# Optimization experiments

Measured on AMD Instinct MI355X. Metric: run time of the kernel, lower is better.

## Reference

```python
import jax, jax.numpy as jnp
import numpy as np


def _conv(x, w, b):
    # PyTorch Conv2d(k=4, s=2, p=1): NCHW x OIHW correlation
    y = jax.lax.conv_general_dilated(x, w, window_strides=(2, 2),
                                     padding=((1, 1), (1, 1)),
                                     dimension_numbers=('NCHW', 'OIHW', 'NCHW'))
    return y + b[None, :, None, None]


def _conv_t(x, w, b):
    # PyTorch ConvTranspose2d(k=4, s=2, p=1); w has torch shape (Cin, Cout, 4, 4).
    # Adjoint of strided correlation = correlation with spatially-flipped,
    # channel-swapped kernel and lhs dilation; pad = k - 1 - p = 2.
    wk = jnp.flip(w, (2, 3)).transpose(1, 0, 2, 3)  # (Cout, Cin, 4, 4)
    y = jax.lax.conv_general_dilated(x, wk, window_strides=(1, 1),
                                     padding=((2, 2), (2, 2)),
                                     lhs_dilation=(2, 2),
                                     dimension_numbers=('NCHW', 'OIHW', 'NCHW'))
    return y + b[None, :, None, None]


def setup_inputs() -> dict:
    key = jax.random.key(0)
    ks = jax.random.split(key, 18)
    s = 0.05
    inp = {'x': jax.random.normal(ks[0], (32, 3, 256, 256), jnp.float32)}
    # encoder weights (OIHW)
    enc_shapes = [(64, 3, 4, 4), (128, 64, 4, 4), (256, 128, 4, 4), (512, 256, 4, 4)]
    for i, sh in enumerate(enc_shapes):
        inp[f'e_w{i+1}'] = jax.random.normal(ks[1 + i], sh, jnp.float32) * s
        inp[f'e_b{i+1}'] = jnp.zeros((sh[0],), jnp.float32)
    # decoder weights (torch ConvTranspose2d layout: Cin, Cout, kH, kW)
    dec_shapes = [(512, 128, 4, 4), (128, 64, 4, 4), (64, 32, 4, 4), (32, 3, 4, 4)]
    for i, sh in enumerate(dec_shapes):
        inp[f'd_w{i+1}'] = jax.random.normal(ks[5 + i], sh, jnp.float32) * s
        inp[f'd_b{i+1}'] = jnp.zeros((sh[1],), jnp.float32)
    # codebook (num_embeddings=1024, embedding_dim=512)
    inp['embed'] = jax.random.normal(ks[9], (1024, 512), jnp.float32)
    return inp


def reference(x, e_w1, e_b1, e_w2, e_b2, e_w3, e_b3, e_w4, e_b4,
              d_w1, d_b1, d_w2, d_b2, d_w3, d_b3, d_w4, d_b4, embed):
    # encoder
    h = jax.nn.relu(_conv(x, e_w1, e_b1))
    h = jax.nn.relu(_conv(h, e_w2, e_b2))
    h = jax.nn.relu(_conv(h, e_w3, e_b3))
    z = jax.nn.relu(_conv(h, e_w4, e_b4))  # (B, 512, 16, 16)
    # quantizer: NCHW -> NHWC -> flat (B*H*W, D)
    B, D, H, W = z.shape
    z_flat = z.transpose(0, 2, 3, 1).reshape(-1, D)
    # squared L2 distance to each code: ||z||^2 - 2 z.E^T + ||E||^2
    dist = (jnp.sum(z_flat ** 2, axis=1, keepdims=True)
            - 2.0 * z_flat @ embed.T
            + jnp.sum(embed ** 2, axis=1))  # (N, K)
    idx = jnp.argmin(dist, axis=1)
    quantized = embed[idx]  # gather == one_hot @ embed
    z_q = quantized.reshape(B, H, W, D).transpose(0, 3, 1, 2)  # NCHW
    # decoder
    h = jax.nn.relu(_conv_t(z_q, d_w1, d_b1))
    h = jax.nn.relu(_conv_t(h, d_w2, d_b2))
    h = jax.nn.relu(_conv_t(h, d_w3, d_b3))
    out = jnp.tanh(_conv_t(h, d_w4, d_b4))  # (B, 3, 256, 256)
    return out
```

## Files before the change

kernel.cpp:

```cpp
#include <hip/hip_runtime.h>
#include <math.h>


typedef __attribute__((ext_vector_type(8))) short bf16x8;
typedef __attribute__((ext_vector_type(4))) float f32x4;
union FragU { unsigned u[4]; bf16x8 v; };

__device__ __forceinline__ unsigned bf16_rne(unsigned u) {
    return (u + 0x7FFFu + ((u >> 16) & 1u)) >> 16;
}
__device__ __forceinline__ unsigned pack_split(float v) {
    unsigned u = __builtin_bit_cast(unsigned, v);
    unsigned hi = bf16_rne(u);
    float hif = __builtin_bit_cast(float, hi << 16);
    float r = v - hif;
    unsigned lo = bf16_rne(__builtin_bit_cast(unsigned, r));
    return hi | (lo << 16);
}

__global__ void __launch_bounds__(256) pack_tensor(
    const float* __restrict__ s, unsigned* __restrict__ d, int n)
{
    int i = blockIdx.x * 256 + threadIdx.x;
    if (i < n) d[i] = pack_split(s[i]);
}

template<int Cin, int Cout>
__global__ void __launch_bounds__(256) repack_wt(
    const float* __restrict__ w, unsigned* __restrict__ wq)
{
    constexpr int TOT = 16 * Cin * Cout;
    int idx = blockIdx.x * 256 + threadIdx.x;
    if (idx >= TOT) return;
    int t  = idx & 3;
    int ci = (idx >> 2) % Cin;
    int rest = (idx >> 2) / Cin;
    int co  = rest % Cout;
    int par = rest / Cout;
    int dy = par >> 1, dx = par & 1;
    int r = t >> 1, s = t & 1;
    int ky = 3 - dy - 2 * r;
    int kx = 3 - dx - 2 * s;
    float v = w[(((size_t)ci * Cout + co) * 4 + ky) * 4 + kx];
    wq[idx] = pack_split(v);
}

__global__ void __launch_bounds__(256) embed_transpose(
    const float* __restrict__ embed, float* __restrict__ et)
{
    int idx = blockIdx.x * 256 + threadIdx.x;
    int c = idx & 1023, k = idx >> 10;
    et[idx] = embed[(size_t)c * 512 + k];
}

template<int Cin, int H, int W, int Cout, int PACKO>
__global__ void __launch_bounds__(256) conv4s2_mfma(
    const unsigned* __restrict__ xp, const unsigned* __restrict__ wp,
    const float* __restrict__ bias, float* __restrict__ y)
{
    constexpr int OH = H / 2, OW = W / 2;
    constexpr int LOG_OW = (OW == 64) ? 6 : (OW == 32) ? 5 : 4;
    constexpr int R   = 64 / OW;
    constexpr int RT  = 2 * R + 2;
    constexpr int CS  = W + 2;
    constexpr int XEL = 2 * RT * CS;
    constexpr int XIT = (XEL + 255) / 256;
    constexpr int K   = Cin * 16;
    constexpr int NC  = Cin / 2;
    constexpr int NB  = 128;
    constexpr int MBC = 32 * OH * OW / 64;

    __shared__ unsigned smem[8704];
    unsigned* raw = smem;
    unsigned* wb  = smem + ((XEL + 7) & ~7);

    int bid = blockIdx.x;
    int mb = bid % MBC, ng = bid / MBC;
    int oc0 = ng * NB;
    int m0 = mb * 64;
    int nimg = m0 / (OH * OW);
    int sp0 = m0 % (OH * OW);
    int oyb = sp0 >> LOG_OW;

    int tid  = threadIdx.x;
    int lane = tid & 63, wv = tid >> 6;
    int lm = lane & 15, q = lane >> 4;
    int n0w = wv * 32;

    const unsigned* xbase = xp + (size_t)nimg * Cin * H * W;

    int  goff[XIT];
    bool gok[XIT];
#pragma unroll
    for (int s = 0; s < XIT; ++s) {
        int i = tid + 256 * s;
        goff[s] = 0; gok[s] = false;
        if (i < XEL) {
            int lc = i % CS;
            int t2 = i / CS;
            int lr = t2 % RT;
            int c  = t2 / RT;
            int gr = 2 * oyb - 1 + lr;
            int gc = lc - 1;
            bool ok = ((unsigned)gr < (unsigned)H) && ((unsigned)gc < (unsigned)W);
            goff[s] = ok ? (c * H * W + gr * W + gc) : 0;
            gok[s]  = ok;
        }
    }
    const unsigned* wbase = wp + (size_t)(oc0 + (tid >> 5)) * K + (tid & 31);
    int wlds0 = (tid >> 5) * 36 + (tid & 31);

    f32x4 acc[4][2];
#pragma unroll
    for (int nt = 0; nt < 2; ++nt) {
        float b = bias[oc0 + n0w + nt * 16 + lm];
#pragma unroll
        for (int mt = 0; mt < 4; ++mt)
#pragma unroll
            for (int r = 0; r < 4; ++r) acc[mt][nt][r] = b;
    }

    unsigned pfa[XIT];
    unsigned pfb[16];

    auto load_chunk = [&](int ch) {
        const unsigned* cb = xbase + (size_t)(ch * 2) * (H * W);
#pragma unroll
        for (int s = 0; s < XIT; ++s) {
            unsigned v = 0;
            if (gok[s]) v = cb[goff[s]];
            pfa[s] = v;
        }
        const unsigned* wc = wbase + ch * 32;
#pragma unroll
        for (int s = 0; s < 16; ++s) pfb[s] = wc[(size_t)s * 8 * K];
    };
    auto store_chunk = [&]() {
#pragma unroll
        for (int s = 0; s < XIT; ++s) {
            int i = tid + 256 * s;
            if (i < XEL) raw[i] = pfa[s];
        }
#pragma unroll
        for (int s = 0; s < 16; ++s) wb[wlds0 + s * 288] = pfb[s];
    };

    load_chunk(0);
#pragma unroll 1
    for (int ch = 0; ch < NC; ++ch) {
        __syncthreads();
        store_chunk();
        __syncthreads();
        if (ch + 1 < NC) load_chunk(ch + 1);

        FragU bhi[2], blo[2];
#pragma unroll
        for (int nt = 0; nt < 2; ++nt) {
            const unsigned* bp = &wb[(n0w + nt * 16 + lm) * 36 + q * 8];
            uint4 p0 = *(const uint4*)bp;
            uint4 p1 = *(const uint4*)(bp + 4);
            unsigned e0 = p0.x, e1 = p0.y, e2 = p0.z, e3 = p0.w;
            unsigned e4 = p1.x, e5 = p1.y, e6 = p1.z, e7 = p1.w;
            bhi[nt].u[0] = (e0 & 0xffffu) | (e1 << 16);
            bhi[nt].u[1] = (e2 & 0xffffu) | (e3 << 16);
            bhi[nt].u[2] = (e4 & 0xffffu) | (e5 << 16);
            bhi[nt].u[3] = (e6 & 0xffffu) | (e7 << 16);
            blo[nt].u[0] = (e0 >> 16) | (e1 & 0xffff0000u);
            blo[nt].u[1] = (e2 >> 16) | (e3 & 0xffff0000u);
            blo[nt].u[2] = (e4 >> 16) | (e5 & 0xffff0000u);
            blo[nt].u[3] = (e6 >> 16) | (e7 & 0xffff0000u);
        }
#pragma unroll
        for (int mt = 0; mt < 4; ++mt) {
            int m = mt * 16 + lm;
            int oyl = m >> LOG_OW, oxl = m & (OW - 1);
            int c = q >> 1, rb = 2 * oyl + (q & 1) * 2;
            const unsigned* rp = &raw[(c * RT + rb) * CS + 2 * oxl];
            uint2 a0 = *(const uint2*)rp;
            uint2 a1 = *(const uint2*)(rp + 2);
            uint2 a2 = *(const uint2*)(rp + CS);
            uint2 a3 = *(const uint2*)(rp + CS + 2);
            FragU ahi, alo;
            ahi.u[0] = (a0.x & 0xffffu) | (a0.y << 16);
            ahi.u[1] = (a1.x & 0xffffu) | (a1.y << 16);
            ahi.u[2] = (a2.x & 0xffffu) | (a2.y << 16);
            ahi.u[3] = (a3.x & 0xffffu) | (a3.y << 16);
            alo.u[0] = (a0.x >> 16) | (a0.y & 0xffff0000u);
            alo.u[1] = (a1.x >> 16) | (a1.y & 0xffff0000u);
            alo.u[2] = (a2.x >> 16) | (a2.y & 0xffff0000u);
            alo.u[3] = (a3.x >> 16) | (a3.y & 0xffff0000u);
#pragma unroll
            for (int nt = 0; nt < 2; ++nt) {
                acc[mt][nt] = __builtin_amdgcn_mfma_f32_16x16x32_bf16(
                    ahi.v, bhi[nt].v, acc[mt][nt], 0, 0, 0);
                acc[mt][nt] = __builtin_amdgcn_mfma_f32_16x16x32_bf16(
                    ahi.v, blo[nt].v, acc[mt][nt], 0, 0, 0);
                acc[mt][nt] = __builtin_amdgcn_mfma_f32_16x16x32_bf16(
                    alo.v, bhi[nt].v, acc[mt][nt], 0, 0, 0);
            }
        }
    }

    __syncthreads();
    float* cs = (float*)smem;
#pragma unroll
    for (int mt = 0; mt < 4; ++mt)
#pragma unroll
        for (int nt = 0; nt < 2; ++nt) {
            int nl = n0w + nt * 16 + lm;
#pragma unroll
            for (int r = 0; r < 4; ++r)
                cs[nl * 68 + mt * 16 + q * 4 + r] = acc[mt][nt][r];
        }
    __syncthreads();
    {
        int nl = tid >> 1, half = tid & 1;
        size_t gb = ((size_t)(nimg * Cout + oc0 + nl)) * (OH * OW) + sp0 + half * 32;
#pragma unroll
        for (int i2 = 0; i2 < 8; ++i2) {
            float4 v = *(float4*)&cs[nl * 68 + half * 32 + 4 * i2];
            v.x = fmaxf(v.x, 0.0f); v.y = fmaxf(v.y, 0.0f);
            v.z = fmaxf(v.z, 0.0f); v.w = fmaxf(v.w, 0.0f);
            if (PACKO) {
                uint4 p;
                p.x = pack_split(v.x); p.y = pack_split(v.y);
                p.z = pack_split(v.z); p.w = pack_split(v.w);
                *(uint4*)((unsigned*)y + gb + 4 * i2) = p;
            } else {
                *(float4*)(y + gb + 4 * i2) = v;
            }
        }
    }
}

template<int Cin, int Hh, int Wh, int Cout, int MT, int NT, int PACKO>
__global__ void __launch_bounds__(256) convt4s2_mfma(
    const unsigned* __restrict__ xp, const unsigned* __restrict__ wq,
    const float* __restrict__ bias, float* __restrict__ y)
{
    constexpr int W = Wh;
    constexpr int LOG_W = (W == 64) ? 6 : (W == 32) ? 5 : 4;
    constexpr int R   = 64 / W;
    constexpr int RT  = R + 1;
    constexpr int CS  = W + 2;
    constexpr int XEL = 8 * RT * CS;
    constexpr int XIT = (XEL + 255) / 256;
    constexpr int K   = Cin * 4;
    constexpr int NC  = Cin / 8;
    constexpr int NB  = Cout;
    constexpr int WIT = NB / 8;
    constexpr int WN  = Cout / (16 * NT);
    constexpr int WM  = 4 / WN;
    static_assert(WM * MT * 16 == 64, "M tiling");
    static_assert(WN * NT * 16 == Cout, "N tiling");
    constexpr int MBC = 32 * Hh * W / 64;
    constexpr int XPAD = (XEL + 7) & ~7;
    constexpr int SM1 = XPAD + NB * 36;
    constexpr int SM2 = NB * 68;
    constexpr int SMEM = SM1 > SM2 ? SM1 : SM2;

    __shared__ unsigned smem[SMEM];
    unsigned* raw = smem;
    unsigned* wb  = smem + XPAD;

    int bid = blockIdx.x;
    int mb  = bid % MBC;
    int par = bid / MBC;
    int dy = par >> 1, dx = par & 1;

    int m0   = mb * 64;
    int nimg = m0 / (Hh * W);
    int sp0  = m0 % (Hh * W);
    int il0  = sp0 >> LOG_W;

    int tid = threadIdx.x;
    int lane = tid & 63, wv = tid >> 6;
    int lm = lane & 15, q = lane >> 4;
    int wm = wv / WN, wn = wv % WN;

    const unsigned* xbase = xp + (size_t)nimg * Cin * Hh * W;

    int  goff[XIT];
    bool gok[XIT];
#pragma unroll
    for (int s = 0; s < XIT; ++s) {
        int i = tid + 256 * s;
        goff[s] = 0; gok[s] = false;
        if (i < XEL) {
            int lc = i % CS;
            int t2 = i / CS;
            int lr = t2 % RT;
            int c  = t2 / RT;
            int gr = il0 - 1 + dy + lr;
            int gc = lc - 1;
            bool ok = ((unsigned)gr < (unsigned)Hh) && ((unsigned)gc < (unsigned)W);
            goff[s] = ok ? (c * Hh * W + gr * W + gc) : 0;
            gok[s]  = ok;
        }
    }
    const unsigned* wbase = wq + (size_t)(par * Cout + (tid >> 5)) * K + (tid & 31);
    int wlds0 = (tid >> 5) * 36 + (tid & 31);

    f32x4 acc[MT][NT];
#pragma unroll
    for (int nt = 0; nt < NT; ++nt) {
        float b = bias[wn * NT * 16 + nt * 16 + lm];
#pragma unroll
        for (int mt = 0; mt < MT; ++mt)
#pragma unroll
            for (int r = 0; r < 4; ++r) acc[mt][nt][r] = b;
    }

    unsigned pfa[XIT];
    unsigned pfb[WIT];

    auto load_chunk = [&](int ch) {
        const unsigned* cb = xbase + (size_t)(ch * 8) * (Hh * W);
#pragma unroll
        for (int s = 0; s < XIT; ++s) {
            unsigned v = 0;
            if (gok[s]) v = cb[goff[s]];
            pfa[s] = v;
        }
        const unsigned* wc = wbase + ch * 32;
#pragma unroll
        for (int s = 0; s < WIT; ++s) pfb[s] = wc[(size_t)s * 8 * K];
    };
    auto store_chunk = [&]() {
#pragma unroll
        for (int s = 0; s < XIT; ++s) {
            int i = tid + 256 * s;
            if (i < XEL) raw[i] = pfa[s];
        }
#pragma unroll
        for (int s = 0; s < WIT; ++s) wb[wlds0 + s * 288] = pfb[s];
    };

    load_chunk(0);
#pragma unroll 1
    for (int ch = 0; ch < NC; ++ch) {
        __syncthreads();
        store_chunk();
        __syncthreads();
        if (ch + 1 < NC) load_chunk(ch + 1);

        FragU bhi[NT], blo[NT];
#pragma unroll
        for (int nt = 0; nt < NT; ++nt) {
            const unsigned* bp = &wb[(wn * NT * 16 + nt * 16 + lm) * 36 + q * 8];
            uint4 p0 = *(const uint4*)bp;
            uint4 p1 = *(const uint4*)(bp + 4);
            unsigned e0 = p0.x, e1 = p0.y, e2 = p0.z, e3 = p0.w;
            unsigned e4 = p1.x, e5 = p1.y, e6 = p1.z, e7 = p1.w;
            bhi[nt].u[0] = (e0 & 0xffffu) | (e1 << 16);
            bhi[nt].u[1] = (e2 & 0xffffu) | (e3 << 16);
            bhi[nt].u[2] = (e4 & 0xffffu) | (e5 << 16);
            bhi[nt].u[3] = (e6 & 0xffffu) | (e7 << 16);
            blo[nt].u[0] = (e0 >> 16) | (e1 & 0xffff0000u);
            blo[nt].u[1] = (e2 >> 16) | (e3 & 0xffff0000u);
            blo[nt].u[2] = (e4 >> 16) | (e5 & 0xffff0000u);
            blo[nt].u[3] = (e6 >> 16) | (e7 & 0xffff0000u);
        }
#pragma unroll
        for (int mt = 0; mt < MT; ++mt) {
            int ml = wm * (MT * 16) + mt * 16 + lm;
            int il = ml >> LOG_W, jl = ml & (W - 1);
            const unsigned* rp = &raw[((2 * q) * RT + il) * CS + jl + dx];
            unsigned a00 = rp[0],               a01 = rp[1];
            unsigned a10 = rp[CS],              a11 = rp[CS + 1];
            unsigned a20 = rp[RT * CS],         a21 = rp[RT * CS + 1];
            unsigned a30 = rp[RT * CS + CS],    a31 = rp[RT * CS + CS + 1];
            FragU ahi, alo;
            ahi.u[0] = (a00 & 0xffffu) | (a01 << 16);
            ahi.u[1] = (a10 & 0xffffu) | (a11 << 16);
            ahi.u[2] = (a20 & 0xffffu) | (a21 << 16);
            ahi.u[3] = (a30 & 0xffffu) | (a31 << 16);
            alo.u[0] = (a00 >> 16) | (a01 & 0xffff0000u);
            alo.u[1] = (a10 >> 16) | (a11 & 0xffff0000u);
            alo.u[2] = (a20 >> 16) | (a21 & 0xffff0000u);
            alo.u[3] = (a30 >> 16) | (a31 & 0xffff0000u);
#pragma unroll
            for (int nt = 0; nt < NT; ++nt) {
                acc[mt][nt] = __builtin_amdgcn_mfma_f32_16x16x32_bf16(
                    ahi.v, bhi[nt].v, acc[mt][nt], 0, 0, 0);
                acc[mt][nt] = __builtin_amdgcn_mfma_f32_16x16x32_bf16(
                    ahi.v, blo[nt].v, acc[mt][nt], 0, 0, 0);
                acc[mt][nt] = __builtin_amdgcn_mfma_f32_16x16x32_bf16(
                    alo.v, bhi[nt].v, acc[mt][nt], 0, 0, 0);
            }
        }
    }

    __syncthreads();
    float* cs = (float*)smem;
#pragma unroll
    for (int mt = 0; mt < MT; ++mt)
#pragma unroll
        for (int nt = 0; nt < NT; ++nt) {
            int nl  = wn * NT * 16 + nt * 16 + lm;
            int mb2 = wm * (MT * 16) + mt * 16 + q * 4;
#pragma unroll
            for (int r = 0; r < 4; ++r)
                cs[nl * 68 + mb2 + r] = acc[mt][nt][r];
        }
    __syncthreads();
    constexpr int EIT = NB * 64 / 256;
#pragma unroll
    for (int it = 0; it < EIT; ++it) {
        int idx = tid + 256 * it;
        int c = idx >> 6, m = idx & 63;
        int il = m >> LOG_W, jl = m & (W - 1);
        int oy = 2 * (il0 + il) + dy;
        int ox = 2 * jl + dx;
        float v = fmaxf(cs[c * 68 + m], 0.0f);
        size_t go = (((size_t)(nimg * Cout + c)) * (2 * Hh) + oy) * (2 * W) + ox;
        if (PACKO) ((unsigned*)y)[go] = pack_split(v);
        else       y[go] = v;
    }
}

template<int Cin, int H, int W, int OCT, int UNR, bool INT>
__device__ __forceinline__ void conv_core(
    const float* __restrict__ xn, const float* __restrict__ wbase,
    int iy0, int ix0, float (&acc)[OCT][4])
{
#pragma unroll UNR
    for (int ic = 0; ic < Cin; ++ic) {
        const float* xc = xn + (size_t)ic * (H * W);
        float xv[4][10];
#pragma unroll
        for (int ky = 0; ky < 4; ++ky) {
            int iy = iy0 + ky;
            if (INT) {
                const float* xr = xc + (size_t)iy * W;
#pragma unroll
                for (int j = 0; j < 10; ++j) xv[ky][j] = xr[ix0 + j];
            } else {
                bool rv = ((unsigned)iy < (unsigned)H);
                const float* xr = xc + (size_t)(rv ? iy : 0) * W;
#pragma unroll
                for (int j = 0; j < 10; ++j) {
                    int ix = ix0 + j;
                    bool cv = rv && ((unsigned)ix < (unsigned)W);
                    xv[ky][j] = cv ? xr[cv ? ix : 0] : 0.0f;
                }
            }
        }
#pragma unroll
        for (int o = 0; o < OCT; ++o) {
            const float* wr = wbase + (size_t)o * (Cin * 16) + ic * 16;
#pragma unroll
            for (int ky = 0; ky < 4; ++ky) {
                float w0 = wr[ky * 4 + 0], w1 = wr[ky * 4 + 1];
                float w2 = wr[ky * 4 + 2], w3 = wr[ky * 4 + 3];
#pragma unroll
                for (int j = 0; j < 4; ++j) {
                    acc[o][j] = fmaf(xv[ky][2 * j],     w0, acc[o][j]);
                    acc[o][j] = fmaf(xv[ky][2 * j + 1], w1, acc[o][j]);
                    acc[o][j] = fmaf(xv[ky][2 * j + 2], w2, acc[o][j]);
                    acc[o][j] = fmaf(xv[ky][2 * j + 3], w3, acc[o][j]);
                }
            }
        }
    }
}

template<int Cin, int H, int W, int Cout, int OCT, int UNR, int PACKO>
__global__ void __launch_bounds__(256) conv4s2_k(
    const float* __restrict__ x, const float* __restrict__ w,
    const float* __restrict__ bias, float* __restrict__ y)
{
    constexpr int OH = H / 2, OW = W / 2, OWq = OW / 4;
    int id = blockIdx.x * 256 + threadIdx.x;
    int ox4 = id % OWq; int t = id / OWq;
    int oy  = t % OH;   t /= OH;
    int ocg = t % (Cout / OCT);
    int n   = t / (Cout / OCT);
    int oc0 = __builtin_amdgcn_readfirstlane(ocg * OCT);
    n       = __builtin_amdgcn_readfirstlane(n);

    float acc[OCT][4];
#pragma unroll
    for (int o = 0; o < OCT; ++o) {
        float b = bias[oc0 + o];
#pragma unroll
        for (int j = 0; j < 4; ++j) acc[o][j] = b;
    }

    const float* xn    = x + (size_t)n * Cin * H * W;
    const float* wbase = w + (size_t)oc0 * Cin * 16;
    int iy0 = 2 * oy - 1;
    int ix0 = 8 * ox4 - 1;

    bool interior = (oy >= 1) && (oy <= OH - 2) && (ox4 >= 1) && (ox4 <= OWq - 2);
    if (interior) conv_core<Cin, H, W, OCT, UNR, true >(xn, wbase, iy0, ix0, acc);
    else          conv_core<Cin, H, W, OCT, UNR, false>(xn, wbase, iy0, ix0, acc);

    int ox0 = ox4 * 4;
#pragma unroll
    for (int o = 0; o < OCT; ++o) {
        size_t gb = (((size_t)n * Cout + oc0 + o) * OH + oy) * OW + ox0;
#pragma unroll
        for (int j = 0; j < 4; ++j) {
            float v = fmaxf(acc[o][j], 0.0f);
            if (PACKO) ((unsigned*)y)[gb + j] = pack_split(v);
            else       y[gb + j] = v;
        }
    }
}

template<int Cin, int H, int W, int Cout, int COT, int ACT, int UNR>
__global__ void __launch_bounds__(256) convt4s2_k(
    const float* __restrict__ x, const float* __restrict__ w,
    const float* __restrict__ bias, float* __restrict__ y)
{
    constexpr int OH = 2 * H, OW = 2 * W, OWq = OW / 4;
    int id = blockIdx.x * 256 + threadIdx.x;
    int ox4 = id % OWq; int t = id / OWq;
    int oy  = t % OH;   t /= OH;
    int cog = t % (Cout / COT);
    int n   = t / (Cout / COT);
    int co0 = __builtin_amdgcn_readfirstlane(cog * COT);
    n       = __builtin_amdgcn_readfirstlane(n);

    int p   = (oy + 1) & 1;
    int iyA = (oy + 1 - p) >> 1;
    int iyB = iyA - 1;
    bool vA = (iyA < H);
    bool vB = (iyB >= 0);
    int iyAc = vA ? iyA : 0, iyBc = vB ? iyB : 0;

    int t0 = 2 * ox4;
    bool c0 = (t0 - 1 >= 0);
    bool c3 = (t0 + 2 <= W - 1);
    int j0 = c0 ? t0 - 1 : 0;
    int j3 = c3 ? t0 + 2 : 0;

    float acc[COT][4];
#pragma unroll
    for (int o = 0; o < COT; ++o) {
        float b = bias[co0 + o];
#pragma unroll
        for (int j = 0; j < 4; ++j) acc[o][j] = b;
    }

    const float* xn = x + (size_t)n * Cin * H * W;

#pragma unroll UNR
    for (int ci = 0; ci < Cin; ++ci) {
        const float* xc  = xn + (size_t)ci * (H * W);
        const float* xrA = xc + (size_t)iyAc * W;
        const float* xrB = xc + (size_t)iyBc * W;
        float a0 = (vA && c0) ? xrA[j0]     : 0.0f;
        float a1 =  vA        ? xrA[t0]     : 0.0f;
        float a2 =  vA        ? xrA[t0 + 1] : 0.0f;
        float a3 = (vA && c3) ? xrA[j3]     : 0.0f;
        float b0 = (vB && c0) ? xrB[j0]     : 0.0f;
        float b1 =  vB        ? xrB[t0]     : 0.0f;
        float b2 =  vB        ? xrB[t0 + 1] : 0.0f;
        float b3 = (vB && c3) ? xrB[j3]     : 0.0f;

        const float* wci = w + ((size_t)ci * Cout + co0) * 16;
#pragma unroll
        for (int o = 0; o < COT; ++o) {
            const float* wr = wci + (size_t)o * 16;
            float wA0 = wr[p * 4 + 0], wA1 = wr[p * 4 + 1];
            float wA2 = wr[p * 4 + 2], wA3 = wr[p * 4 + 3];
            float wB0 = wr[(p + 2) * 4 + 0], wB1 = wr[(p + 2) * 4 + 1];
            float wB2 = wr[(p + 2) * 4 + 2], wB3 = wr[(p + 2) * 4 + 3];
            acc[o][0] = fmaf(a1, wA1, acc[o][0]); acc[o][0] = fmaf(a0, wA3, acc[o][0]);
            acc[o][0] = fmaf(b1, wB1, acc[o][0]); acc[o][0] = fmaf(b0, wB3, acc[o][0]);
            acc[o][1] = fmaf(a2, wA0, acc[o][1]); acc[o][1] = fmaf(a1, wA2, acc[o][1]);
            acc[o][1] = fmaf(b2, wB0, acc[o][1]); acc[o][1] = fmaf(b1, wB2, acc[o][1]);
            acc[o][2] = fmaf(a2, wA1, acc[o][2]); acc[o][2] = fmaf(a1, wA3, acc[o][2]);
            acc[o][2] = fmaf(b2, wB1, acc[o][2]); acc[o][2] = fmaf(b1, wB3, acc[o][2]);
            acc[o][3] = fmaf(a3, wA0, acc[o][3]); acc[o][3] = fmaf(a2, wA2, acc[o][3]);
            acc[o][3] = fmaf(b3, wB0, acc[o][3]); acc[o][3] = fmaf(b2, wB2, acc[o][3]);
        }
    }

    int ox0 = ox4 * 4;
#pragma unroll
    for (int o = 0; o < COT; ++o) {
        float* yr = y + (((size_t)n * Cout + co0 + o) * OH + oy) * OW + ox0;
#pragma unroll
        for (int j = 0; j < 4; ++j) {
            float v = acc[o][j];
            yr[j] = (ACT == 0) ? fmaxf(v, 0.0f) : tanhf(v);
        }
    }
}

__global__ void __launch_bounds__(256) embed_norms(
    const float* __restrict__ embed, float* __restrict__ norms)
{
    int c = blockIdx.x * 256 + threadIdx.x;
    const float* e = embed + (size_t)c * 512;
    float s = 0.0f;
    for (int k = 0; k < 512; ++k) s = fmaf(e[k], e[k], s);
    norms[c] = s;
}

__global__ void __launch_bounds__(256) vq_argmin16(
    const float* __restrict__ z, const float* __restrict__ et,
    const float* __restrict__ norms, int* __restrict__ out)
{
    constexpr int ZS = 516;
    int row0 = blockIdx.x * 16;
    int n    = row0 >> 8;
    int yx0  = row0 & 255;
    int tid  = threadIdx.x;

    __shared__ float zr[16 * ZS];

    const float* zn = z + ((size_t)n * 512) * 256;
#pragma unroll
    for (int it = 0; it < 8; ++it) {
        int i  = tid + 256 * it;
        int rq = i & 3, kc = i >> 2;
        float4 v = *(const float4*)&zn[(size_t)kc * 256 + yx0 + 4 * rq];
        zr[(4 * rq + 0) * ZS + kc] = v.x;
        zr[(4 * rq + 1) * ZS + kc] = v.y;
        zr[(4 * rq + 2) * ZS + kc] = v.z;
        zr[(4 * rq + 3) * ZS + kc] = v.w;
    }
    __syncthreads();

    float acc[16][4];
#pragma unroll
    for (int r = 0; r < 16; ++r)
#pragma unroll
        for (int j = 0; j < 4; ++j) acc[r][j] = 0.0f;

    const float* ebase = et + 4 * tid;
#pragma unroll 1
    for (int k4 = 0; k4 < 128; ++k4) {
        float4 e0 = *(const float4*)&ebase[(size_t)(4 * k4 + 0) * 1024];
        float4 e1 = *(const float4*)&ebase[(size_t)(4 * k4 + 1) * 1024];
        float4 e2 = *(const float4*)&ebase[(size_t)(4 * k4 + 2) * 1024];
        float4 e3 = *(const float4*)&ebase[(size_t)(4 * k4 + 3) * 1024];
#pragma unroll
        for (int r = 0; r < 16; ++r) {
            float4 zz = *(const float4*)&zr[r * ZS + 4 * k4];
            float a0 = acc[r][0], a1 = acc[r][1], a2 = acc[r][2], a3 = acc[r][3];
            a0 = fmaf(zz.x, e0.x, a0); a0 = fmaf(zz.y, e1.x, a0);
            a0 = fmaf(zz.z, e2.x, a0); a0 = fmaf(zz.w, e3.x, a0);
            a1 = fmaf(zz.x, e0.y, a1); a1 = fmaf(zz.y, e1.y, a1);
            a1 = fmaf(zz.z, e2.y, a1); a1 = fmaf(zz.w, e3.y, a1);
            a2 = fmaf(zz.x, e0.z, a2); a2 = fmaf(zz.y, e1.z, a2);
            a2 = fmaf(zz.z, e2.z, a2); a2 = fmaf(zz.w, e3.z, a2);
            a3 = fmaf(zz.x, e0.w, a3); a3 = fmaf(zz.y, e1.w, a3);
            a3 = fmaf(zz.z, e2.w, a3); a3 = fmaf(zz.w, e3.w, a3);
            acc[r][0] = a0; acc[r][1] = a1; acc[r][2] = a2; acc[r][3] = a3;
        }
    }

    float4 nb = *(const float4*)&norms[4 * tid];
    float best[16]; int bi[16];
#pragma unroll
    for (int r = 0; r < 16; ++r) {
        float d0 = nb.x - 2.0f * acc[r][0];
        float d1 = nb.y - 2.0f * acc[r][1];
        float d2 = nb.z - 2.0f * acc[r][2];
        float d3 = nb.w - 2.0f * acc[r][3];
        float b = d0; int ix = 4 * tid;
        if (d1 < b) { b = d1; ix = 4 * tid + 1; }
        if (d2 < b) { b = d2; ix = 4 * tid + 2; }
        if (d3 < b) { b = d3; ix = 4 * tid + 3; }
        best[r] = b; bi[r] = ix;
    }

    __syncthreads();
    float* rbd = zr;
    int*   rbi = (int*)(zr + 4096);
#pragma unroll
    for (int r = 0; r < 16; ++r) {
        rbd[r * 256 + tid] = best[r];
        rbi[r * 256 + tid] = bi[r];
    }
    __syncthreads();
    for (int s = 128; s > 0; s >>= 1) {
        if (tid < s) {
#pragma unroll
            for (int r = 0; r < 16; ++r) {
                int i0 = r * 256 + tid;
                float od = rbd[i0 + s]; int oi = rbi[i0 + s];
                float md = rbd[i0];     int mi = rbi[i0];
                if (od < md || (od == md && oi < mi)) { rbd[i0] = od; rbi[i0] = oi; }
            }
        }
        __syncthreads();
    }
    if (tid < 16) out[row0 + tid] = rbi[tid * 256];
}

__global__ void __launch_bounds__(256) vq_gather_pack(
    const int* __restrict__ vidx, const float* __restrict__ embed,
    unsigned* __restrict__ zq)
{
    int i = blockIdx.x * 256 + threadIdx.x;
    int yx = i & 255;
    int t  = i >> 8;
    int c  = t & 511;
    int n  = t >> 9;
    int row = (n << 8) + yx;
    zq[i] = pack_split(embed[(size_t)vidx[row] * 512 + c]);
}

extern "C" void kernel_launch(void* const* d_in, const int* in_sizes, int n_in,
                              void* d_out, int out_size, void* d_ws, size_t ws_size,
                              hipStream_t stream)
{
    (void)in_sizes; (void)n_in; (void)out_size; (void)ws_size;
    const float* x     = (const float*)d_in[0];
    const float* ew1   = (const float*)d_in[1];
    const float* eb1   = (const float*)d_in[2];
    const float* ew2   = (const float*)d_in[3];
    const float* eb2   = (const float*)d_in[4];
    const float* ew3   = (const float*)d_in[5];
    const float* eb3   = (const float*)d_in[6];
    const float* ew4   = (const float*)d_in[7];
    const float* eb4   = (const float*)d_in[8];
    const float* dw1   = (const float*)d_in[9];
    const float* db1   = (const float*)d_in[10];
    const float* dw2   = (const float*)d_in[11];
    const float* db2   = (const float*)d_in[12];
    const float* dw3   = (const float*)d_in[13];
    const float* db3   = (const float*)d_in[14];
    const float* dw4   = (const float*)d_in[15];
    const float* db4   = (const float*)d_in[16];
    const float* embed = (const float*)d_in[17];
    float* out = (float*)d_out;

    unsigned* W0   = (unsigned*)d_ws;
    unsigned* h1p  = W0;
    unsigned* h2p  = W0 + 33554432;
    unsigned* h3p  = W0;
    float*    z    = (float*)(W0 + 8388608);
    unsigned* zq   = W0 + 12582912;
    float*    P0   = (float*)(W0 + 16777216);
    float*    P1   = (float*)(W0 + 20971520);
    int*      vidx = (int*)(W0 + 29360128);
    float*    norms= (float*)(W0 + 29368320);
    float*    g3o  = (float*)h2p;

    unsigned* wp2 = (unsigned*)d_out;
    unsigned* wp3 = wp2 + 131072;
    unsigned* wp4 = wp2 + 655360;
    unsigned* wq1 = wp2 + 2752512;
    unsigned* wq2 = wq1 + 1048576;
    unsigned* wq3 = wq2 + 131072;
    float*    et  = (float*)(wq3 + 32768);

    dim3 b256(256);

    pack_tensor<<<dim3(512),  b256, 0, stream>>>(ew2, wp2, 131072);
    pack_tensor<<<dim3(2048), b256, 0, stream>>>(ew3, wp3, 524288);
    pack_tensor<<<dim3(8192), b256, 0, stream>>>(ew4, wp4, 2097152);
    repack_wt<512, 128><<<dim3(4096), b256, 0, stream>>>(dw1, wq1);
    repack_wt<128,  64><<<dim3(512),  b256, 0, stream>>>(dw2, wq2);
    repack_wt< 64,  32><<<dim3(128),  b256, 0, stream>>>(dw3, wq3);
    embed_transpose<<<dim3(2048), b256, 0, stream>>>(embed, et);

    conv4s2_k<3, 256, 256, 64, 4, 3, 1><<<dim3(8192), b256, 0, stream>>>(
        x, ew1, eb1, (float*)h1p);
    conv4s2_mfma<64, 128, 128, 128, 1><<<dim3(2048), b256, 0, stream>>>(
        h1p, wp2, eb2, (float*)h2p);
    conv4s2_mfma<128, 64, 64, 256, 1><<<dim3(1024), b256, 0, stream>>>(
        h2p, wp3, eb3, (float*)h3p);
    conv4s2_mfma<256, 32, 32, 512, 0><<<dim3(512), b256, 0, stream>>>(
        h3p, wp4, eb4, z);

    embed_norms<<<dim3(4), b256, 0, stream>>>(embed, norms);
    vq_argmin16<<<dim3(512), b256, 0, stream>>>(z, et, norms, vidx);
    vq_gather_pack<<<dim3(16384), b256, 0, stream>>>(vidx, embed, zq);

    convt4s2_mfma<512, 16, 16, 128, 4, 2, 1><<<dim3(4 * 128), b256, 0, stream>>>(
        zq, wq1, db1, P0);
    convt4s2_mfma<128, 32, 32, 64, 4, 1, 1><<<dim3(4 * 512), b256, 0, stream>>>(
        (const unsigned*)P0, wq2, db2, P1);
    convt4s2_mfma<64, 64, 64, 32, 2, 1, 0><<<dim3(4 * 2048), b256, 0, stream>>>(
        (const unsigned*)P1, wq3, db3, g3o);
    convt4s2_k<32, 128, 128, 3, 3, 1, 2><<<dim3(2048), b256, 0, stream>>>(
        g3o, dw4, db4, out);
}
```

Baseline: 1.272 ms.

## Run first encoder conv on MFMA with split-bf16 packed input

Replaces the scalar FMA first encoder convolution (Cin=3) with a generalized MFMA implicit-GEMM kernel that pads Cin to 4, packs the input image and weights into hi/lo bf16 pairs, and uses three bf16 MFMAs per tile to approximate fp32. This aims to move the large 256x256 first layer onto matrix cores instead of vector ALUs. It adds an extra full-input packing pass over x and wastes a quarter of the K dimension on zero padding.

```diff
diff --git a/kernel.cpp b/kernel.cpp
--- a/kernel.cpp
+++ b/kernel.cpp
@@ -23,6 +23,16 @@
 {
     int i = blockIdx.x * 256 + threadIdx.x;
     if (i < n) d[i] = pack_split(s[i]);
+}
+
+__global__ void __launch_bounds__(256) pack_w1(
+    const float* __restrict__ w, unsigned* __restrict__ wq)
+{
+    int idx = blockIdx.x * 256 + threadIdx.x;
+    if (idx >= 64 * 64) return;
+    int k = idx & 63, oc = idx >> 6;
+    float v = (k < 48) ? w[oc * 48 + k] : 0.0f;
+    wq[idx] = pack_split(v);
 }
 
 template<int Cin, int Cout>
@@ -219,6 +229,204 @@
 #pragma unroll
         for (int i2 = 0; i2 < 8; ++i2) {
             float4 v = *(float4*)&cs[nl * 68 + half * 32 + 4 * i2];
+            v.x = fmaxf(v.x, 0.0f); v.y = fmaxf(v.y, 0.0f);
+            v.z = fmaxf(v.z, 0.0f); v.w = fmaxf(v.w, 0.0f);
+            if (PACKO) {
+                uint4 p;
+                p.x = pack_split(v.x); p.y = pack_split(v.y);
+                p.z = pack_split(v.z); p.w = pack_split(v.w);
+                *(uint4*)((unsigned*)y + gb + 4 * i2) = p;
+            } else {
+                *(float4*)(y + gb + 4 * i2) = v;
+            }
+        }
+    }
+}
+
+template<int Cin, int CINR, int H, int W, int Cout, int MT, int NT, int PACKO>
+__global__ void __launch_bounds__(256) conv4s2_mfma_g(
+    const unsigned* __restrict__ xp, const unsigned* __restrict__ wp,
+    const float* __restrict__ bias, float* __restrict__ y)
+{
+    constexpr int OH = H / 2, OW = W / 2;
+    constexpr int OWB = (OW >= 64) ? 64 : OW;
+    constexpr int LOG_OWB = (OWB == 64) ? 6 : (OWB == 32) ? 5 : 4;
+    constexpr int LOG_OW  = (OW == 128) ? 7 : (OW == 64) ? 6 : (OW == 32) ? 5 : 4;
+    constexpr int R   = 64 / OWB;
+    constexpr int RT  = 2 * R + 2;
+    constexpr int CS  = 2 * OWB + 2;
+    constexpr int XEL = 2 * RT * CS;
+    constexpr int XIT = (XEL + 255) / 256;
+    constexpr int K   = Cin * 16;
+    constexpr int NC  = Cin / 2;
+    constexpr int NB  = Cout;
+    constexpr int WIT = NB / 8;
+    constexpr int WN  = Cout / (16 * NT);
+    constexpr int WM  = 4 / WN;
+    static_assert(WM * MT * 16 == 64, "M tiling");
+    static_assert(WN * NT * 16 == Cout, "N tiling");
+    constexpr int MBC = 32 * OH * OW / 64;
+    constexpr int XPAD = (XEL + 7) & ~7;
+    constexpr int SM1 = XPAD + NB * 36;
+    constexpr int SM2 = NB * 68;
+    constexpr int SMEM = SM1 > SM2 ? SM1 : SM2;
+
+    __shared__ unsigned smem[SMEM];
+    unsigned* raw = smem;
+    unsigned* wb  = smem + XPAD;
+
+    int bid = blockIdx.x;
+    int mb = bid % MBC, ng = bid / MBC;
+    int oc0 = ng * NB;
+    int m0 = mb * 64;
+    int nimg = m0 / (OH * OW);
+    int sp0 = m0 % (OH * OW);
+    int oyb = sp0 >> LOG_OW;
+    int oxb = sp0 & (OW - 1);
+
+    int tid  = threadIdx.x;
+    int lane = tid & 63, wv = tid >> 6;
+    int lm = lane & 15, q = lane >> 4;
+    int wm = wv / WN, wn = wv % WN;
+
+    const unsigned* xbase = xp + (size_t)nimg * CINR * H * W;
+
+    int  goff[XIT];
+    bool gok[XIT];
+    int  cidx[XIT];
+#pragma unroll
+    for (int s = 0; s < XIT; ++s) {
+        int i = tid + 256 * s;
+        goff[s] = 0; gok[s] = false; cidx[s] = 0;
+        if (i < XEL) {
+            int lc = i % CS;
+            int t2 = i / CS;
+            int lr = t2 % RT;
+            int c  = t2 / RT;
+            int gr = 2 * oyb - 1 + lr;
+            int gc = 2 * oxb - 1 + lc;
+            bool ok = ((unsigned)gr < (unsigned)H) && ((unsigned)gc < (unsigned)W);
+            goff[s] = ok ? (c * H * W + gr * W + gc) : 0;
+            gok[s]  = ok;
+            cidx[s] = c;
+        }
+    }
+    const unsigned* wbase = wp + (size_t)(oc0 + (tid >> 5)) * K + (tid & 31);
+    int wlds0 = (tid >> 5) * 36 + (tid & 31);
+
+    f32x4 acc[MT][NT];
+#pragma unroll
+    for (int nt = 0; nt < NT; ++nt) {
+        float b = bias[oc0 + wn * NT * 16 + nt * 16 + lm];
+#pragma unroll
+        for (int mt = 0; mt < MT; ++mt)
+#pragma unroll
+            for (int r = 0; r < 4; ++r) acc[mt][nt][r] = b;
+    }
+
+    unsigned pfa[XIT];
+    unsigned pfb[WIT];
+
+    auto load_chunk = [&](int ch) {
+        const unsigned* cb = xbase + (size_t)(ch * 2) * (H * W);
+#pragma unroll
+        for (int s = 0; s < XIT; ++s) {
+            unsigned v = 0;
+            bool okc = (2 * ch + cidx[s]) < CINR;
+            if (gok[s] && okc) v = cb[goff[s]];
+            pfa[s] = v;
+        }
+        const unsigned* wc = wbase + ch * 32;
+#pragma unroll
+        for (int s = 0; s < WIT; ++s) pfb[s] = wc[(size_t)s * 8 * K];
+    };
+    auto store_chunk = [&]() {
+#pragma unroll
+        for (int s = 0; s < XIT; ++s) {
+            int i = tid + 256 * s;
+            if (i < XEL) raw[i] = pfa[s];
+        }
+#pragma unroll
+        for (int s = 0; s < WIT; ++s) wb[wlds0 + s * 288] = pfb[s];
+    };
+
+    load_chunk(0);
+#pragma unroll 1
+    for (int ch = 0; ch < NC; ++ch) {
+        __syncthreads();
+        store_chunk();
+        __syncthreads();
+        if (ch + 1 < NC) load_chunk(ch + 1);
+
+        FragU bhi[NT], blo[NT];
+#pragma unroll
+        for (int nt = 0; nt < NT; ++nt) {
+            const unsigned* bp = &wb[(wn * NT * 16 + nt * 16 + lm) * 36 + q * 8];
+            uint4 p0 = *(const uint4*)bp;
+            uint4 p1 = *(const uint4*)(bp + 4);
+            unsigned e0 = p0.x, e1 = p0.y, e2 = p0.z, e3 = p0.w;
+            unsigned e4 = p1.x, e5 = p1.y, e6 = p1.z, e7 = p1.w;
+            bhi[nt].u[0] = (e0 & 0xffffu) | (e1 << 16);
+            bhi[nt].u[1] = (e2 & 0xffffu) | (e3 << 16);
+            bhi[nt].u[2] = (e4 & 0xffffu) | (e5 << 16);
+            bhi[nt].u[3] = (e6 & 0xffffu) | (e7 << 16);
+            blo[nt].u[0] = (e0 >> 16) | (e1 & 0xffff0000u);
+            blo[nt].u[1] = (e2 >> 16) | (e3 & 0xffff0000u);
+            blo[nt].u[2] = (e4 >> 16) | (e5 & 0xffff0000u);
+            blo[nt].u[3] = (e6 >> 16) | (e7 & 0xffff0000u);
+        }
+#pragma unroll
+        for (int mt = 0; mt < MT; ++mt) {
+            int m = wm * (MT * 16) + mt * 16 + lm;
+            int oyl = m >> LOG_OWB, oxl = m & (OWB - 1);
+            int c = q >> 1, rb = 2 * oyl + (q & 1) * 2;
+            const unsigned* rp = &raw[(c * RT + rb) * CS + 2 * oxl];
+            uint2 a0 = *(const uint2*)rp;
+            uint2 a1 = *(const uint2*)(rp + 2);
+            uint2 a2 = *(const uint2*)(rp + CS);
+            uint2 a3 = *(const uint2*)(rp + CS + 2);
+            FragU ahi, alo;
+            ahi.u[0] = (a0.x & 0xffffu) | (a0.y << 16);
+            ahi.u[1] = (a1.x & 0xffffu) | (a1.y << 16);
+            ahi.u[2] = (a2.x & 0xffffu) | (a2.y << 16);
+            ahi.u[3] = (a3.x & 0xffffu) | (a3.y << 16);
+            alo.u[0] = (a0.x >> 16) | (a0.y & 0xffff0000u);
+            alo.u[1] = (a1.x >> 16) | (a1.y & 0xffff0000u);
+            alo.u[2] = (a2.x >> 16) | (a2.y & 0xffff0000u);
+            alo.u[3] = (a3.x >> 16) | (a3.y & 0xffff0000u);
+#pragma unroll
+            for (int nt = 0; nt < NT; ++nt) {
+                acc[mt][nt] = __builtin_amdgcn_mfma_f32_16x16x32_bf16(
+                    ahi.v, bhi[nt].v, acc[mt][nt], 0, 0, 0);
+                acc[mt][nt] = __builtin_amdgcn_mfma_f32_16x16x32_bf16(
+                    ahi.v, blo[nt].v, acc[mt][nt], 0, 0, 0);
+                acc[mt][nt] = __builtin_amdgcn_mfma_f32_16x16x32_bf16(
+                    alo.v, bhi[nt].v, acc[mt][nt], 0, 0, 0);
+            }
+        }
+    }
+
+    __syncthreads();
+    float* cs = (float*)smem;
+#pragma unroll
+    for (int mt = 0; mt < MT; ++mt)
+#pragma unroll
+        for (int nt = 0; nt < NT; ++nt) {
+            int nl  = wn * NT * 16 + nt * 16 + lm;
+            int mb2 = wm * (MT * 16) + mt * 16 + q * 4;
+#pragma unroll
+            for (int r = 0; r < 4; ++r)
+                cs[nl * 68 + mb2 + r] = acc[mt][nt][r];
+        }
+    __syncthreads();
+    {
+        constexpr int QT = 256 / NB;
+        int nl = tid / QT, qt = tid % QT;
+        constexpr int MQ = 64 / QT;
+        size_t gb = ((size_t)(nimg * Cout + oc0 + nl)) * (OH * OW) + sp0 + qt * MQ;
+#pragma unroll
+        for (int i2 = 0; i2 < MQ / 4; ++i2) {
+            float4 v = *(float4*)&cs[nl * 68 + qt * MQ + 4 * i2];
             v.x = fmaxf(v.x, 0.0f); v.y = fmaxf(v.y, 0.0f);
             v.z = fmaxf(v.z, 0.0f); v.w = fmaxf(v.w, 0.0f);
             if (PACKO) {
@@ -419,96 +627,6 @@
     }
 }
 
-template<int Cin, int H, int W, int OCT, int UNR, bool INT>
-__device__ __forceinline__ void conv_core(
-    const float* __restrict__ xn, const float* __restrict__ wbase,
-    int iy0, int ix0, float (&acc)[OCT][4])
-{
-#pragma unroll UNR
-    for (int ic = 0; ic < Cin; ++ic) {
-        const float* xc = xn + (size_t)ic * (H * W);
-        float xv[4][10];
-#pragma unroll
-        for (int ky = 0; ky < 4; ++ky) {
-            int iy = iy0 + ky;
-            if (INT) {
-                const float* xr = xc + (size_t)iy * W;
-#pragma unroll
-                for (int j = 0; j < 10; ++j) xv[ky][j] = xr[ix0 + j];
-            } else {
-                bool rv = ((unsigned)iy < (unsigned)H);
-                const float* xr = xc + (size_t)(rv ? iy : 0) * W;
-#pragma unroll
-                for (int j = 0; j < 10; ++j) {
-                    int ix = ix0 + j;
-                    bool cv = rv && ((unsigned)ix < (unsigned)W);
-                    xv[ky][j] = cv ? xr[cv ? ix : 0] : 0.0f;
-                }
-            }
-        }
-#pragma unroll
-        for (int o = 0; o < OCT; ++o) {
-            const float* wr = wbase + (size_t)o * (Cin * 16) + ic * 16;
-#pragma unroll
-            for (int ky = 0; ky < 4; ++ky) {
-                float w0 = wr[ky * 4 + 0], w1 = wr[ky * 4 + 1];
-                float w2 = wr[ky * 4 + 2], w3 = wr[ky * 4 + 3];
-#pragma unroll
-                for (int j = 0; j < 4; ++j) {
-                    acc[o][j] = fmaf(xv[ky][2 * j],     w0, acc[o][j]);
-                    acc[o][j] = fmaf(xv[ky][2 * j + 1], w1, acc[o][j]);
-                    acc[o][j] = fmaf(xv[ky][2 * j + 2], w2, acc[o][j]);
-                    acc[o][j] = fmaf(xv[ky][2 * j + 3], w3, acc[o][j]);
-                }
-            }
-        }
-    }
-}
-
-template<int Cin, int H, int W, int Cout, int OCT, int UNR, int PACKO>
-__global__ void __launch_bounds__(256) conv4s2_k(
-    const float* __restrict__ x, const float* __restrict__ w,
-    const float* __restrict__ bias, float* __restrict__ y)
-{
-    constexpr int OH = H / 2, OW = W / 2, OWq = OW / 4;
-    int id = blockIdx.x * 256 + threadIdx.x;
-    int ox4 = id % OWq; int t = id / OWq;
-    int oy  = t % OH;   t /= OH;
-    int ocg = t % (Cout / OCT);
-    int n   = t / (Cout / OCT);
-    int oc0 = __builtin_amdgcn_readfirstlane(ocg * OCT);
-    n       = __builtin_amdgcn_readfirstlane(n);
-
-    float acc[OCT][4];
-#pragma unroll
-    for (int o = 0; o < OCT; ++o) {
-        float b = bias[oc0 + o];
-#pragma unroll
-        for (int j = 0; j < 4; ++j) acc[o][j] = b;
-    }
-
-    const float* xn    = x + (size_t)n * Cin * H * W;
-    const float* wbase = w + (size_t)oc0 * Cin * 16;
-    int iy0 = 2 * oy - 1;
-    int ix0 = 8 * ox4 - 1;
-
-    bool interior = (oy >= 1) && (oy <= OH - 2) && (ox4 >= 1) && (ox4 <= OWq - 2);
-    if (interior) conv_core<Cin, H, W, OCT, UNR, true >(xn, wbase, iy0, ix0, acc);
-    else          conv_core<Cin, H, W, OCT, UNR, false>(xn, wbase, iy0, ix0, acc);
-
-    int ox0 = ox4 * 4;
-#pragma unroll
-    for (int o = 0; o < OCT; ++o) {
-        size_t gb = (((size_t)n * Cout + oc0 + o) * OH + oy) * OW + ox0;
-#pragma unroll
-        for (int j = 0; j < 4; ++j) {
-            float v = fmaxf(acc[o][j], 0.0f);
-            if (PACKO) ((unsigned*)y)[gb + j] = pack_split(v);
-            else       y[gb + j] = v;
-        }
-    }
-}
-
 template<int Cin, int H, int W, int Cout, int COT, int ACT, int UNR>
 __global__ void __launch_bounds__(256) convt4s2_k(
     const float* __restrict__ x, const float* __restrict__ w,
@@ -735,6 +853,7 @@
     unsigned* W0   = (unsigned*)d_ws;
     unsigned* h1p  = W0;
     unsigned* h2p  = W0 + 33554432;
+    unsigned* xp1  = W0 + 33554432;
     unsigned* h3p  = W0;
     float*    z    = (float*)(W0 + 8388608);
     unsigned* zq   = W0 + 12582912;
@@ -751,19 +870,22 @@
     unsigned* wq2 = wq1 + 1048576;
     unsigned* wq3 = wq2 + 131072;
     float*    et  = (float*)(wq3 + 32768);
+    unsigned* wp1 = (unsigned*)(et + 524288);
 
     dim3 b256(256);
 
     pack_tensor<<<dim3(512),  b256, 0, stream>>>(ew2, wp2, 131072);
     pack_tensor<<<dim3(2048), b256, 0, stream>>>(ew3, wp3, 524288);
     pack_tensor<<<dim3(8192), b256, 0, stream>>>(ew4, wp4, 2097152);
+    pack_w1<<<dim3(16), b256, 0, stream>>>(ew1, wp1);
+    pack_tensor<<<dim3(24576), b256, 0, stream>>>(x, xp1, 6291456);
     repack_wt<512, 128><<<dim3(4096), b256, 0, stream>>>(dw1, wq1);
     repack_wt<128,  64><<<dim3(512),  b256, 0, stream>>>(dw2, wq2);
     repack_wt< 64,  32><<<dim3(128),  b256, 0, stream>>>(dw3, wq3);
     embed_transpose<<<dim3(2048), b256, 0, stream>>>(embed, et);
 
-    conv4s2_k<3, 256, 256, 64, 4, 3, 1><<<dim3(8192), b256, 0, stream>>>(
-        x, ew1, eb1, (float*)h1p);
+    conv4s2_mfma_g<4, 3, 256, 256, 64, 4, 1, 1><<<dim3(8192), b256, 0, stream>>>(
+        xp1, wp1, eb1, (float*)h1p);
     conv4s2_mfma<64, 128, 128, 128, 1><<<dim3(2048), b256, 0, stream>>>(
         h1p, wp2, eb2, (float*)h2p);
     conv4s2_mfma<128, 64, 64, 256, 1><<<dim3(1024), b256, 0, stream>>>(
```

Measured after the change: 1.167 ms. 1.09x faster.
